# Kernel optimization log

Measured on AMD Instinct MI355X. Metric: run time of the kernel, lower is better.

Reference implementation:

```python
import jax, jax.numpy as jnp
import numpy as np

TEMP = 0.05


def _l2norm(x, axis=-1, eps=1e-12):
    n = jnp.sqrt(jnp.sum(x * x, axis=axis, keepdims=True))
    return x / jnp.maximum(n, eps)


def setup_inputs() -> dict:
    key = jax.random.key(0)
    k1, k2, k3 = jax.random.split(key, 3)
    B, D, N = 1024, 2048, 16384
    inputs = jax.random.normal(k1, (B, D), dtype=jnp.float32)
    targets = jax.random.randint(k2, (B,), 0, N, dtype=jnp.int32).astype(jnp.int64)
    # cluster memory bank: initialized to unit-norm centroids (buffer is zeros in
    # torch but is always filled with normalized centroids before use)
    features = _l2norm(jax.random.normal(k3, (N, D), dtype=jnp.float32))
    return {"inputs": inputs, "targets": targets, "features": features}


def reference(inputs, targets, features):
    # ClusterMemory.forward: normalize -> cosine sim vs bank -> / temp
    xn = _l2norm(inputs, axis=1)            # [B, D]
    out = (xn @ features.T) / TEMP          # [B, N]
    return out
```

## Files before the change

kernel.cpp:

```cpp
#include <hip/hip_runtime.h>
#include <hip/hip_bf16.h>


typedef short bf16x8 __attribute__((ext_vector_type(8)));
typedef float f32x4  __attribute__((ext_vector_type(4)));

#define D_K   2048
#define N_N   16384
#define M_M   1024
#define TEMP_INV 20.0f

__device__ __forceinline__ unsigned short f2bf(float f) {
    unsigned u = __builtin_bit_cast(unsigned, f);
    u += 0x7FFFu + ((u >> 16) & 1u);
    return (unsigned short)(u >> 16);
}

#define GLOAD16(g, l) __builtin_amdgcn_global_load_lds(                        \
    (const __attribute__((address_space(1))) unsigned int*)(g),                \
    (__attribute__((address_space(3))) unsigned int*)(l), 16, 0, 0)

__global__ __launch_bounds__(256) void anorm_kernel(const float* __restrict__ x,
                                                    unsigned short* __restrict__ abf) {
    int row = blockIdx.x;
    int t = threadIdx.x;
    const float4* xr = reinterpret_cast<const float4*>(x + (size_t)row * D_K);
    float4 a = xr[t * 2];
    float4 b = xr[t * 2 + 1];
    float s = a.x*a.x + a.y*a.y + a.z*a.z + a.w*a.w
            + b.x*b.x + b.y*b.y + b.z*b.z + b.w*b.w;
    #pragma unroll
    for (int off = 32; off > 0; off >>= 1) s += __shfl_down(s, off);
    __shared__ float ps[4];
    __shared__ float sbc;
    if ((t & 63) == 0) ps[t >> 6] = s;
    __syncthreads();
    if (t == 0) {
        float tot = ps[0] + ps[1] + ps[2] + ps[3];
        sbc = 1.0f / fmaxf(sqrtf(tot), 1e-12f);
    }
    __syncthreads();
    float rs = sbc;
    bf16x8 v;
    v[0] = (short)f2bf(a.x * rs); v[1] = (short)f2bf(a.y * rs);
    v[2] = (short)f2bf(a.z * rs); v[3] = (short)f2bf(a.w * rs);
    v[4] = (short)f2bf(b.x * rs); v[5] = (short)f2bf(b.y * rs);
    v[6] = (short)f2bf(b.z * rs); v[7] = (short)f2bf(b.w * rs);
    *reinterpret_cast<bf16x8*>(abf + (size_t)row * D_K + t * 8) = v;
}

__global__ __launch_bounds__(256) void bconv_kernel(const float* __restrict__ B,
                                                    unsigned short* __restrict__ bbf) {
    const size_t nv = (size_t)N_N * D_K / 8;
    size_t stride = (size_t)gridDim.x * blockDim.x;
    for (size_t v = (size_t)blockIdx.x * blockDim.x + threadIdx.x; v < nv; v += stride) {
        const float4* p = reinterpret_cast<const float4*>(B) + v * 2;
        float4 a = p[0], b = p[1];
        bf16x8 o;
        o[0] = (short)f2bf(a.x); o[1] = (short)f2bf(a.y);
        o[2] = (short)f2bf(a.z); o[3] = (short)f2bf(a.w);
        o[4] = (short)f2bf(b.x); o[5] = (short)f2bf(b.y);
        o[6] = (short)f2bf(b.z); o[7] = (short)f2bf(b.w);
        reinterpret_cast<bf16x8*>(bbf)[v] = o;
    }
}

__global__ __launch_bounds__(256, 4) void gemm_bf_kernel(const unsigned short* __restrict__ Abf,
                                                         const unsigned short* __restrict__ Bbf,
                                                         float* __restrict__ C) {
    __shared__ __align__(16) unsigned short lA[128 * 64];
    __shared__ __align__(16) unsigned short lB[128 * 64];

    int bid = blockIdx.x;
    int wg  = (bid & 7) * 128 + (bid >> 3);
    int tm  = wg & 7, tn = wg >> 3;
    int m0 = tm * 128, n0 = tn * 128;

    int t = threadIdx.x, lane = t & 63, w = t >> 6;
    int wr = (w >> 1) * 64, wc = (w & 1) * 64;

    const unsigned short* ga[4];
    const unsigned short* gb[4];
    unsigned lo[4];
    #pragma unroll
    for (int j = 0; j < 4; ++j) {
        int row = j * 32 + w * 8 + (lane >> 3);
        int ss  = (lane & 7) ^ (row & 7);
        ga[j] = Abf + (size_t)(m0 + row) * D_K + ss * 8;
        gb[j] = Bbf + (size_t)(n0 + row) * D_K + ss * 8;
        lo[j] = (unsigned)(j * 4096 + w * 1024);
    }

    f32x4 acc[4][4] = {};

    for (int kt = 0; kt < D_K / 64; ++kt) {
        if (kt) __syncthreads();
        int k0 = kt * 64;
        #pragma unroll
        for (int j = 0; j < 4; ++j) {
            GLOAD16(ga[j] + k0, (char*)lA + lo[j]);
            GLOAD16(gb[j] + k0, (char*)lB + lo[j]);
        }
        __syncthreads();
        #pragma unroll
        for (int ks = 0; ks < 2; ++ks) {
            bf16x8 af[4], bfr[4];
            #pragma unroll
            for (int f = 0; f < 4; ++f) {
                int ar = wr + f * 16 + (lane & 15);
                int as = (ks * 4 + (lane >> 4)) ^ (ar & 7);
                af[f] = *reinterpret_cast<const bf16x8*>(&lA[ar * 64 + as * 8]);
                int br = wc + f * 16 + (lane & 15);
                int bs = (ks * 4 + (lane >> 4)) ^ (br & 7);
                bfr[f] = *reinterpret_cast<const bf16x8*>(&lB[br * 64 + bs * 8]);
            }
            #pragma unroll
            for (int m = 0; m < 4; ++m)
                #pragma unroll
                for (int n = 0; n < 4; ++n)
                    acc[m][n] = __builtin_amdgcn_mfma_f32_16x16x32_bf16(
                        af[m], bfr[n], acc[m][n], 0, 0, 0);
        }
    }

    #pragma unroll
    for (int m = 0; m < 4; ++m) {
        int r = m0 + wr + m * 16 + (lane >> 4) * 4;
        #pragma unroll
        for (int j = 0; j < 4; ++j) {
            float* cp = C + (size_t)(r + j) * N_N + n0 + wc + (lane & 15);
            #pragma unroll
            for (int n = 0; n < 4; ++n)
                cp[n * 16] = acc[m][n][j] * TEMP_INV;
        }
    }
}

__global__ __launch_bounds__(256) void rnorm_kernel(const float* __restrict__ x,
                                                    float* __restrict__ rn) {
    int row = blockIdx.x;
    const float4* xr = reinterpret_cast<const float4*>(x + (size_t)row * D_K);
    int t = threadIdx.x;
    float4 a = xr[t];
    float4 b = xr[t + 256];
    float s = a.x*a.x + a.y*a.y + a.z*a.z + a.w*a.w
            + b.x*b.x + b.y*b.y + b.z*b.z + b.w*b.w;
    #pragma unroll
    for (int off = 32; off > 0; off >>= 1) s += __shfl_down(s, off);
    __shared__ float ps[4];
    int wave = t >> 6, lane = t & 63;
    if (lane == 0) ps[wave] = s;
    __syncthreads();
    if (t == 0) {
        float tot = ps[0] + ps[1] + ps[2] + ps[3];
        rn[row] = 1.0f / fmaxf(sqrtf(tot), 1e-12f);
    }
}

__global__ __launch_bounds__(256, 2) void gemm_kernel(const float* __restrict__ A,
                                                      const float* __restrict__ Bm,
                                                      const float* __restrict__ rn,
                                                      float* __restrict__ C) {
    constexpr int BK = 64;
    __shared__ __align__(16) short lAs[128 * BK];
    __shared__ __align__(16) short lBs[128 * BK];
    int bid = blockIdx.x;
    int nb  = (bid & 7) * 128 + (bid >> 3);
    int tm  = nb & 7;
    int tn  = nb >> 3;
    int m0 = tm * 128, n0 = tn * 128;
    int t = threadIdx.x;
    int lane = t & 63, w = t >> 6;
    int wr = (w >> 1) * 64, wc = (w & 1) * 64;
    f32x4 acc[4][4] = {};
    float4 ra[4][2], rb[4][2];
    float  sc[4];
    int    srow[4], sgrp[4];
    #pragma unroll
    for (int i = 0; i < 4; ++i) {
        int li = t + i * 256;
        srow[i] = li >> 3;
        sgrp[i] = li & 7;
        sc[i]   = rn[m0 + srow[i]];
    }
    auto load_tiles = [&](int kt) {
        int k0 = kt * BK;
        #pragma unroll
        for (int i = 0; i < 4; ++i) {
            const float4* pa = reinterpret_cast<const float4*>(
                A + (size_t)(m0 + srow[i]) * D_K + k0 + sgrp[i] * 8);
            ra[i][0] = pa[0]; ra[i][1] = pa[1];
            const float4* pb = reinterpret_cast<const float4*>(
                Bm + (size_t)(n0 + srow[i]) * D_K + k0 + sgrp[i] * 8);
            rb[i][0] = pb[0]; rb[i][1] = pb[1];
        }
    };
    auto write_tiles = [&]() {
        #pragma unroll
        for (int i = 0; i < 4; ++i) {
            int row = srow[i];
            int slot = sgrp[i] ^ (row & 7);
            float s = sc[i];
            bf16x8 va, vb;
            va[0] = (short)f2bf(ra[i][0].x * s); va[1] = (short)f2bf(ra[i][0].y * s);
            va[2] = (short)f2bf(ra[i][0].z * s); va[3] = (short)f2bf(ra[i][0].w * s);
            va[4] = (short)f2bf(ra[i][1].x * s); va[5] = (short)f2bf(ra[i][1].y * s);
            va[6] = (short)f2bf(ra[i][1].z * s); va[7] = (short)f2bf(ra[i][1].w * s);
            vb[0] = (short)f2bf(rb[i][0].x); vb[1] = (short)f2bf(rb[i][0].y);
            vb[2] = (short)f2bf(rb[i][0].z); vb[3] = (short)f2bf(rb[i][0].w);
            vb[4] = (short)f2bf(rb[i][1].x); vb[5] = (short)f2bf(rb[i][1].y);
            vb[6] = (short)f2bf(rb[i][1].z); vb[7] = (short)f2bf(rb[i][1].w);
            *reinterpret_cast<bf16x8*>(&lAs[row * BK + slot * 8]) = va;
            *reinterpret_cast<bf16x8*>(&lBs[row * BK + slot * 8]) = vb;
        }
    };
    auto compute = [&]() {
        #pragma unroll
        for (int ks = 0; ks < 2; ++ks) {
            bf16x8 af[4], bfr[4];
            #pragma unroll
            for (int f = 0; f < 4; ++f) {
                int arow = wr + f * 16 + (lane & 15);
                int aslot = (ks * 4 + (lane >> 4)) ^ (arow & 7);
                af[f] = *reinterpret_cast<const bf16x8*>(&lAs[arow * BK + aslot * 8]);
                int brow = wc + f * 16 + (lane & 15);
                int bslot = (ks * 4 + (lane >> 4)) ^ (brow & 7);
                bfr[f] = *reinterpret_cast<const bf16x8*>(&lBs[brow * BK + bslot * 8]);
            }
            #pragma unroll
            for (int m = 0; m < 4; ++m)
                #pragma unroll
                for (int n = 0; n < 4; ++n)
                    acc[m][n] = __builtin_amdgcn_mfma_f32_16x16x32_bf16(
                        af[m], bfr[n], acc[m][n], 0, 0, 0);
        }
    };
    load_tiles(0);
    write_tiles();
    for (int kt = 1; kt < D_K / BK; ++kt) {
        __syncthreads();
        load_tiles(kt);
        compute();
        __syncthreads();
        write_tiles();
    }
    __syncthreads();
    compute();
    #pragma unroll
    for (int m = 0; m < 4; ++m) {
        int r = m0 + wr + m * 16 + (lane >> 4) * 4;
        #pragma unroll
        for (int j = 0; j < 4; ++j) {
            float* cp = C + (size_t)(r + j) * N_N + n0 + wc + (lane & 15);
            #pragma unroll
            for (int n = 0; n < 4; ++n)
                cp[n * 16] = acc[m][n][j] * TEMP_INV;
        }
    }
}

extern "C" void kernel_launch(void* const* d_in, const int* in_sizes, int n_in,
                              void* d_out, int out_size, void* d_ws, size_t ws_size,
                              hipStream_t stream) {
    const float* inputs   = (const float*)d_in[0];
    const float* features = (const float*)d_in[2];
    float* out = (float*)d_out;

    const size_t needA = (size_t)M_M * D_K * 2;
    const size_t needB = (size_t)N_N * D_K * 2;
    if (ws_size >= needA + needB) {
        unsigned short* Abf = (unsigned short*)d_ws;
        unsigned short* Bbf = Abf + (size_t)M_M * D_K;
        anorm_kernel<<<M_M, 256, 0, stream>>>(inputs, Abf);
        bconv_kernel<<<2048, 256, 0, stream>>>(features, Bbf);
        gemm_bf_kernel<<<(M_M / 128) * (N_N / 128), 256, 0, stream>>>(Abf, Bbf, out);
    } else {
        float* rn = (float*)d_ws;
        rnorm_kernel<<<M_M, 256, 0, stream>>>(inputs, rn);
        gemm_kernel<<<(M_M / 128) * (N_N / 128), 256, 0, stream>>>(inputs, features, rn, out);
    }
}
```

Measured before the change: 113.0 us.

## Replace bf16 GEMM with 256x256 tile, 8-wave, double-buffered pipelined kernel

Replaces the 128x128 single-buffered bf16 GEMM with a 256x256 tile kernel using 8 waves and a 128KB LDS double buffer. Global-to-LDS loads for later k-slices are issued in interleaved phases alongside MFMA compute, using explicit barriers, vmcnt waits and setprio. This targets the load/compute serialization and the low data reuse of the old kernel. In exchange it uses far more LDS and registers per block, leaving fewer blocks per CU, and relies on hand-tuned waitcnt ordering that could be fragile.

Measured after the change: 108.0 us. 4.4% less time.

```diff
diff --git a/kernel.cpp b/kernel.cpp
--- a/kernel.cpp
+++ b/kernel.cpp
@@ -65,73 +65,110 @@
     }
 }
 
-__global__ __launch_bounds__(256, 4) void gemm_bf_kernel(const unsigned short* __restrict__ Abf,
-                                                         const unsigned short* __restrict__ Bbf,
-                                                         float* __restrict__ C) {
-    __shared__ __align__(16) unsigned short lA[128 * 64];
-    __shared__ __align__(16) unsigned short lB[128 * 64];
+__global__ __launch_bounds__(512, 2) void gemm8_kernel(const unsigned short* __restrict__ Abf,
+                                                       const unsigned short* __restrict__ Bbf,
+                                                       float* __restrict__ C) {
+    __shared__ __align__(16) unsigned short lds[65536];
 
     int bid = blockIdx.x;
-    int wg  = (bid & 7) * 128 + (bid >> 3);
-    int tm  = wg & 7, tn = wg >> 3;
-    int m0 = tm * 128, n0 = tn * 128;
+    int wg  = (bid & 7) * 32 + (bid >> 3);
+    int tm  = wg & 3, tn = wg >> 2;
+    int m_blk = tm * 256, n_blk = tn * 256;
 
     int t = threadIdx.x, lane = t & 63, w = t >> 6;
-    int wr = (w >> 1) * 64, wc = (w & 1) * 64;
-
-    const unsigned short* ga[4];
-    const unsigned short* gb[4];
-    unsigned lo[4];
-    #pragma unroll
-    for (int j = 0; j < 4; ++j) {
-        int row = j * 32 + w * 8 + (lane >> 3);
-        int ss  = (lane & 7) ^ (row & 7);
-        ga[j] = Abf + (size_t)(m0 + row) * D_K + ss * 8;
-        gb[j] = Bbf + (size_t)(n0 + row) * D_K + ss * 8;
-        lo[j] = (unsigned)(j * 4096 + w * 1024);
-    }
-
-    f32x4 acc[4][4] = {};
-
-    for (int kt = 0; kt < D_K / 64; ++kt) {
-        if (kt) __syncthreads();
-        int k0 = kt * 64;
+    int wm = w >> 2, wn = w & 3;
+
+    int l15  = lane & 15;
+    int slot = ((lane >> 4) ^ ((l15 >> 1) & 3)) * 16;
+    int aoff = (wm * 128 + l15) * 64 + slot;
+    int boff = (wn * 64  + l15) * 64 + slot;
+
+    const unsigned short* gA[2];
+    const unsigned short* gB[2];
+    int sdst[2];
+    #pragma unroll
+    for (int pass = 0; pass < 2; ++pass) {
+        int r = pass * 128 + (t >> 2);
+        int csrc = (t & 3) ^ ((r >> 1) & 3);
+        gA[pass] = Abf + (size_t)(m_blk + r) * D_K + csrc * 8;
+        gB[pass] = Bbf + (size_t)(n_blk + r) * D_K + csrc * 8;
+        sdst[pass] = pass * 8192 + w * 1024;
+    }
+
+    auto stage = [&](int mat, int s, int b, int ktile) {
+        int kt = ktile < 32 ? ktile : 31;
+        int koff = kt * 64 + s * 32;
+        int ldsb = b * 65536 + mat * 32768 + s * 16384;
+        GLOAD16((mat ? gB[0] : gA[0]) + koff, (char*)lds + ldsb + sdst[0]);
+        GLOAD16((mat ? gB[1] : gA[1]) + koff, (char*)lds + ldsb + sdst[1]);
+    };
+
+    f32x4 acc[8][4] = {};
+    bf16x8 bfr[4];
+
+#define PHASE(b, mh, s, LOADB, stMat, stS, stB, stKt, VM)                      \
+    {                                                                          \
+        bf16x8 af[4];                                                          \
+        _Pragma("unroll")                                                      \
+        for (int f = 0; f < 4; ++f)                                            \
+            af[f] = *reinterpret_cast<const bf16x8*>(                          \
+                (char*)lds + (b) * 65536 + (s) * 16384 + aoff +                \
+                ((mh) * 64 + f * 16) * 64);                                    \
+        if (LOADB) {                                                           \
+            _Pragma("unroll")                                                  \
+            for (int n = 0; n < 4; ++n)                                        \
+                bfr[n] = *reinterpret_cast<const bf16x8*>(                     \
+                    (char*)lds + (b) * 65536 + 32768 + (s) * 16384 + boff +    \
+                    n * 1024);                                                 \
+        }                                                                      \
+        stage(stMat, stS, stB, stKt);                                          \
+        asm volatile("s_barrier" ::: "memory");                                \
+        asm volatile("s_waitcnt lgkmcnt(0)" ::: "memory");                     \
+        __builtin_amdgcn_sched_barrier(0);                                     \
+        __builtin_amdgcn_s_setprio(1);                                         \
+        _Pragma("unroll")                                                      \
+        for (int f = 0; f < 4; ++f) {                                          \
+            _Pragma("unroll")                                                  \
+            for (int n = 0; n < 4; ++n)                                        \
+                acc[(mh) * 4 + f][n] = __builtin_amdgcn_mfma_f32_16x16x32_bf16(\
+                    af[f], bfr[n], acc[(mh) * 4 + f][n], 0, 0, 0);             \
+        }                                                                      \
+        __builtin_amdgcn_s_setprio(0);                                         \
+        if (VM) asm volatile("s_waitcnt vmcnt(8)" ::: "memory");               \
+        asm volatile("s_barrier" ::: "memory");                                \
+    }
+
+    stage(0, 0, 0, 0);
+    stage(1, 0, 0, 0);
+    stage(0, 1, 0, 0);
+    stage(1, 1, 0, 0);
+    stage(0, 0, 1, 1);
+    stage(1, 0, 1, 1);
+    asm volatile("s_waitcnt vmcnt(8)" ::: "memory");
+    asm volatile("s_barrier" ::: "memory");
+
+    for (int u = 0; u < 16; ++u) {
+        int t1 = 2 * u + 1;
+        PHASE(0, 0, 0, true,  0, 1, 1, t1,     false)
+        PHASE(0, 1, 0, false, 1, 1, 1, t1,     true )
+        PHASE(0, 0, 1, true,  0, 0, 0, t1 + 1, false)
+        PHASE(0, 1, 1, false, 1, 0, 0, t1 + 1, true )
+        PHASE(1, 0, 0, true,  0, 1, 0, t1 + 1, false)
+        PHASE(1, 1, 0, false, 1, 1, 0, t1 + 1, true )
+        PHASE(1, 0, 1, true,  0, 0, 1, t1 + 2, false)
+        PHASE(1, 1, 1, false, 1, 0, 1, t1 + 2, true )
+    }
+#undef PHASE
+
+    #pragma unroll
+    for (int f = 0; f < 8; ++f) {
+        int r = m_blk + wm * 128 + (f >> 2) * 64 + (f & 3) * 16 + (lane >> 4) * 4;
         #pragma unroll
         for (int j = 0; j < 4; ++j) {
-            GLOAD16(ga[j] + k0, (char*)lA + lo[j]);
-            GLOAD16(gb[j] + k0, (char*)lB + lo[j]);
-        }
-        __syncthreads();
-        #pragma unroll
-        for (int ks = 0; ks < 2; ++ks) {
-            bf16x8 af[4], bfr[4];
-            #pragma unroll
-            for (int f = 0; f < 4; ++f) {
-                int ar = wr + f * 16 + (lane & 15);
-                int as = (ks * 4 + (lane >> 4)) ^ (ar & 7);
-                af[f] = *reinterpret_cast<const bf16x8*>(&lA[ar * 64 + as * 8]);
-                int br = wc + f * 16 + (lane & 15);
-                int bs = (ks * 4 + (lane >> 4)) ^ (br & 7);
-                bfr[f] = *reinterpret_cast<const bf16x8*>(&lB[br * 64 + bs * 8]);
-            }
-            #pragma unroll
-            for (int m = 0; m < 4; ++m)
-                #pragma unroll
-                for (int n = 0; n < 4; ++n)
-                    acc[m][n] = __builtin_amdgcn_mfma_f32_16x16x32_bf16(
-                        af[m], bfr[n], acc[m][n], 0, 0, 0);
-        }
-    }
-
-    #pragma unroll
-    for (int m = 0; m < 4; ++m) {
-        int r = m0 + wr + m * 16 + (lane >> 4) * 4;
-        #pragma unroll
-        for (int j = 0; j < 4; ++j) {
-            float* cp = C + (size_t)(r + j) * N_N + n0 + wc + (lane & 15);
+            float* cp = C + (size_t)(r + j) * N_N + n_blk + wn * 64 + (lane & 15);
             #pragma unroll
             for (int n = 0; n < 4; ++n)
-                cp[n * 16] = acc[m][n][j] * TEMP_INV;
+                cp[n * 16] = acc[f][n][j] * TEMP_INV;
         }
     }
 }
@@ -273,7 +310,7 @@
         unsigned short* Bbf = Abf + (size_t)M_M * D_K;
         anorm_kernel<<<M_M, 256, 0, stream>>>(inputs, Abf);
         bconv_kernel<<<2048, 256, 0, stream>>>(features, Bbf);
-        gemm_bf_kernel<<<(M_M / 128) * (N_N / 128), 256, 0, stream>>>(Abf, Bbf, out);
+        gemm8_kernel<<<(M_M / 256) * (N_N / 256), 512, 0, stream>>>(Abf, Bbf, out);
     } else {
         float* rn = (float*)d_ws;
         rnorm_kernel<<<M_M, 256, 0, stream>>>(inputs, rn);
```
